# Kernel tuning notes

Hardware: AMD Instinct MI355X
Metric: run time of the kernel (lower is better)

## Reference

```python
import jax, jax.numpy as jnp
import numpy as np

B, LQ, LK, QD, KD, VD, H = 8, 128, 1024, 128, 128, 128, 128
NEG_INF = -1e6  # d2l masked_softmax fill value


def setup_inputs() -> dict:
    key = jax.random.key(0)
    k1, k2, k3, k4, k5, k6, k7 = jax.random.split(key, 7)
    return {
        "queries": jax.random.normal(k1, (B, LQ, QD), dtype=jnp.float32),
        "keys": jax.random.normal(k2, (B, LK, KD), dtype=jnp.float32),
        "values": jax.random.normal(k3, (B, LK, VD), dtype=jnp.float32),
        "valid_lens": jax.random.randint(k4, (B,), 0, LK),
        # learned params: torch Linear(in,out,bias=False); stored here as [in,out]
        "W_q": jax.random.normal(k5, (QD, H), dtype=jnp.float32) / np.sqrt(QD),
        "W_k": jax.random.normal(k6, (KD, H), dtype=jnp.float32) / np.sqrt(KD),
        "w_v": jax.random.normal(k7, (H,), dtype=jnp.float32) / np.sqrt(H),
    }


def reference(queries, keys, values, valid_lens, W_q, W_k, w_v):
    q = jnp.einsum("blq,qh->blh", queries, W_q)            # [B,Lq,H]
    k = jnp.einsum("bsk,kh->bsh", keys, W_k)               # [B,Lk,H]
    features = jnp.tanh(q[:, :, None, :] + k[:, None, :, :])  # [B,Lq,Lk,H]
    scores = jnp.einsum("blsh,h->bls", features, w_v)      # [B,Lq,Lk]
    mask = jnp.arange(LK)[None, None, :] < valid_lens[:, None, None]
    scores = jnp.where(mask, scores, NEG_INF)
    attn = jax.nn.softmax(scores, axis=-1)                 # dropout p=0.0 -> identity
    return jnp.einsum("bls,bsv->blv", attn, values)        # [B,Lq,Vd]
```

## Files before the change

### kernel.cpp

```cpp
#include <hip/hip_runtime.h>
#include <hip/hip_fp16.h>

#define B_   8
#define LQ_  128
#define LK_  1024
#define H_   128

__device__ float        g_eq  [B_ * LQ_ * H_];
__device__ uint4        g_ekT4[B_ * (H_ / 4) * (LK_ / 2)];
__device__ unsigned int g_vh  [B_ * LK_ * (H_ / 2)];

#define C2LOG2E 2.8853900817779268f

__global__ __launch_bounds__(256) void proj_conv(const float* __restrict__ q,
                                                 const float* __restrict__ k,
                                                 const float* __restrict__ Wq,
                                                 const float* __restrict__ Wk,
                                                 const float* __restrict__ values) {
    const int bx = blockIdx.x, ch = blockIdx.y;
    const int t = threadIdx.x;
    if (bx >= 288) {
        const int idx = ((bx - 288) + (ch << 9)) * 256 + t;
        float4 v = *(const float4*)(values + (size_t)idx * 4);
        __half2 p0 = __floats2half2_rn(v.x, v.y);
        __half2 p1 = __floats2half2_rn(v.z, v.w);
        *(uint2*)(g_vh + (size_t)idx * 2) =
            make_uint2(*(unsigned int*)&p0, *(unsigned int*)&p1);
        return;
    }
    __shared__ float Ws[H_ * 64];
    __shared__ float Xs[32 * H_];
    const bool isq = (bx < 32);
    const float* X; const float* W; int r0;
    if (isq) { X = q; W = Wq; r0 = bx * 32; }
    else     { X = k; W = Wk; r0 = (bx - 32) * 32; }

    #pragma unroll
    for (int u = 0; u < 8; ++u) {
        int p = u * 256 + t;
        int kk = p >> 4, c4 = p & 15;
        *(float4*)(Ws + kk * 64 + c4 * 4) = *(const float4*)(W + kk * H_ + ch * 64 + c4 * 4);
    }
    #pragma unroll
    for (int u = 0; u < 4; ++u) {
        int idx = u * 256 + t;
        int r = idx >> 5, c = idx & 31;
        *(float4*)(Xs + r * H_ + c * 4) = *(const float4*)(X + (size_t)(r0 + r) * H_ + c * 4);
    }
    __syncthreads();

    const int rr = t >> 4;
    const int cc = t & 15;
    float acc[2][4] = {};
    #pragma unroll 4
    for (int kk = 0; kk < H_; ++kk) {
        float4 w4 = *(const float4*)(Ws + kk * 64 + cc * 4);
        float x0 = Xs[(rr * 2) * H_ + kk];
        float x1 = Xs[(rr * 2 + 1) * H_ + kk];
        acc[0][0] = fmaf(x0, w4.x, acc[0][0]); acc[0][1] = fmaf(x0, w4.y, acc[0][1]);
        acc[0][2] = fmaf(x0, w4.z, acc[0][2]); acc[0][3] = fmaf(x0, w4.w, acc[0][3]);
        acc[1][0] = fmaf(x1, w4.x, acc[1][0]); acc[1][1] = fmaf(x1, w4.y, acc[1][1]);
        acc[1][2] = fmaf(x1, w4.z, acc[1][2]); acc[1][3] = fmaf(x1, w4.w, acc[1][3]);
    }
    if (isq) {
        #pragma unroll
        for (int i = 0; i < 2; ++i) {
            float4 o;
            o.x = __builtin_amdgcn_exp2f(acc[i][0] * C2LOG2E);
            o.y = __builtin_amdgcn_exp2f(acc[i][1] * C2LOG2E);
            o.z = __builtin_amdgcn_exp2f(acc[i][2] * C2LOG2E);
            o.w = __builtin_amdgcn_exp2f(acc[i][3] * C2LOG2E);
            *(float4*)(g_eq + (size_t)(r0 + rr * 2 + i) * H_ + ch * 64 + cc * 4) = o;
        }
    } else {
        const int b  = r0 >> 10;
        const int s0 = (r0 & 1023) + rr * 2;
        const int h4 = ch * 16 + cc;
        uint4 pk;
        #pragma unroll
        for (int j = 0; j < 4; ++j) {
            float e0 = __builtin_amdgcn_exp2f(acc[0][j] * C2LOG2E);
            float e1 = __builtin_amdgcn_exp2f(acc[1][j] * C2LOG2E);
            __half2 p = __floats2half2_rn(e0, e1);
            ((unsigned int*)&pk)[j] = *(unsigned int*)&p;
        }
        g_ekT4[((size_t)b * (H_ / 4) + h4) * (LK_ / 2) + (s0 >> 1)] = pk;
    }
}

__global__ __launch_bounds__(512, 2) void fused_attn(const int* __restrict__ valid_lens,
                                                     const float* __restrict__ w_v,
                                                     float* __restrict__ out) {
    __shared__ float qs[2][H_];
    __shared__ float wv[H_];
    __shared__ float scA[LK_], scB[LK_];
    __shared__ float sredA[8], sredB[8];
    __shared__ float rinvs[2];
    __shared__ float part[16][2][H_];
    const int t = threadIdx.x;
    const int lane = t & 63, wid = t >> 6;
    const int g = blockIdx.x & 1;
    const int idx = blockIdx.x >> 1;
    const int b = 4 * g + (idx & 3);
    const int l0 = (idx >> 2) * 2;
    int valid = valid_lens[b];
    valid = min(max(valid, 0), LK_);

    if (t < 256) qs[t >> 7][t & 127] = g_eq[(size_t)(b * LQ_ + l0 + (t >> 7)) * H_ + (t & 127)];
    else if (t < 384) wv[t - 256] = w_v[t - 256];
    __syncthreads();

    const int s0 = 2 * t;
    float p0 = 0.0f, p1 = 0.0f;
    if (valid == 0) {
        for (int i = t; i < LK_; i += 512) { scA[i] = 1.0f; scB[i] = 1.0f; }
    } else if (s0 < valid) {
        const uint4* __restrict__ ek = g_ekT4 + (size_t)b * (H_ / 4) * (LK_ / 2) + t;
        float a00 = 0.0f, a01 = 0.0f, a10 = 0.0f, a11 = 0.0f;
        #pragma unroll 4
        for (int h4 = 0; h4 < H_ / 4; ++h4) {
            uint4 u = ek[(size_t)h4 * (LK_ / 2)];
            #pragma unroll
            for (int j = 0; j < 4; ++j) {
                unsigned int uj = ((const unsigned int*)&u)[j];
                float2 ef = __half22float2(*(const __half2*)&uj);
                const int h = h4 * 4 + j;
                const float qa = qs[0][h], qb = qs[1][h], wh = wv[h];
                a00 = fmaf(wh, __builtin_amdgcn_rcpf(fmaf(qa, ef.x, 1.0f)), a00);
                a01 = fmaf(wh, __builtin_amdgcn_rcpf(fmaf(qa, ef.y, 1.0f)), a01);
                a10 = fmaf(wh, __builtin_amdgcn_rcpf(fmaf(qb, ef.x, 1.0f)), a10);
                a11 = fmaf(wh, __builtin_amdgcn_rcpf(fmaf(qb, ef.y, 1.0f)), a11);
            }
        }
        const float cc = -2.0f * 1.44269504f;
        float e00 = __builtin_amdgcn_exp2f(a00 * cc);
        float e01 = __builtin_amdgcn_exp2f(a01 * cc);
        float e10 = __builtin_amdgcn_exp2f(a10 * cc);
        float e11 = __builtin_amdgcn_exp2f(a11 * cc);
        *(float2*)(scA + s0) = make_float2(e00, e01);
        *(float2*)(scB + s0) = make_float2(e10, e11);
        const bool odd_ok = (s0 + 1 < valid);
        p0 = e00 + (odd_ok ? e01 : 0.0f);
        p1 = e10 + (odd_ok ? e11 : 0.0f);
    }
    #pragma unroll
    for (int kk = 32; kk; kk >>= 1) {
        p0 += __shfl_xor(p0, kk, 64);
        p1 += __shfl_xor(p1, kk, 64);
    }
    if (lane == 0) { sredA[wid] = p0; sredB[wid] = p1; }
    __syncthreads();
    if (t < 2) {
        const float* sr = t ? sredB : sredA;
        float s8 = ((sr[0] + sr[1]) + (sr[2] + sr[3]))
                 + ((sr[4] + sr[5]) + (sr[6] + sr[7]));
        rinvs[t] = (valid == 0) ? (1.0f / 1024.0f) : (1.0f / s8);
    }
    __syncthreads();
    const int n = (valid == 0) ? LK_ : valid;

    const int c = t >> 5;
    const int v4 = t & 31;
    const uint2* vb = (const uint2*)g_vh + (size_t)b * LK_ * (H_ / 4) + v4;
    float ax0 = 0.0f, ay0 = 0.0f, az0 = 0.0f, aw0 = 0.0f;
    float ax1 = 0.0f, ay1 = 0.0f, az1 = 0.0f, aw1 = 0.0f;
    #pragma unroll 4
    for (int s = c; s < n; s += 16) {
        uint2 u = vb[(size_t)s * (H_ / 4)];
        float2 v01 = __half22float2(*(const __half2*)&u.x);
        float2 v23 = __half22float2(*(const __half2*)&u.y);
        float w0 = scA[s], w1 = scB[s];
        ax0 = fmaf(w0, v01.x, ax0); ay0 = fmaf(w0, v01.y, ay0);
        az0 = fmaf(w0, v23.x, az0); aw0 = fmaf(w0, v23.y, aw0);
        ax1 = fmaf(w1, v01.x, ax1); ay1 = fmaf(w1, v01.y, ay1);
        az1 = fmaf(w1, v23.x, az1); aw1 = fmaf(w1, v23.y, aw1);
    }
    *(float4*)(&part[c][0][4 * v4]) = make_float4(ax0, ay0, az0, aw0);
    *(float4*)(&part[c][1][4 * v4]) = make_float4(ax1, ay1, az1, aw1);
    __syncthreads();
    if (t < 256) {
        const int rr = t >> 7, v = t & 127;
        float o = 0.0f;
        #pragma unroll
        for (int cc2 = 0; cc2 < 16; ++cc2) o += part[cc2][rr][v];
        out[(size_t)(b * LQ_ + l0 + rr) * H_ + v] = o * rinvs[rr];
    }
}

extern "C" void kernel_launch(void* const* d_in, const int* in_sizes, int n_in,
                              void* d_out, int out_size, void* d_ws, size_t ws_size,
                              hipStream_t stream) {
    const float* queries    = (const float*)d_in[0];
    const float* keys       = (const float*)d_in[1];
    const float* values     = (const float*)d_in[2];
    const int*   valid_lens = (const int*)d_in[3];
    const float* W_q        = (const float*)d_in[4];
    const float* W_k        = (const float*)d_in[5];
    const float* w_v        = (const float*)d_in[6];
    float* out = (float*)d_out;
    (void)d_ws; (void)ws_size; (void)in_sizes; (void)n_in; (void)out_size;

    proj_conv <<<dim3(800, 2), 256, 0, stream>>>(queries, keys, W_q, W_k, values);
    fused_attn<<<512, 512, 0, stream>>>(valid_lens, w_v, out);
}
```

Measured before the change: 36.97 us.

## Split fused attention into separate score and softmax-PV kernels

Breaks the fused attention kernel into a score kernel and a softmax/PV kernel. The score kernel uses one 128-thread block per query row and 256-key chunk and exits early past valid_len, so load balances across the ragged valid lengths. Scores go through a global buffer that the second kernel reads back into shared memory for the reduction and the PV product. This adds an extra launch and a global round trip for the scores, and each score thread now covers only one query row, so it loses the reuse of each key load across two rows.

Measured after the change: 38.02 us. 1.03x slower.

```diff
diff --git a/kernel.cpp b/kernel.cpp
--- a/kernel.cpp
+++ b/kernel.cpp
@@ -9,6 +9,7 @@
 __device__ float        g_eq  [B_ * LQ_ * H_];
 __device__ uint4        g_ekT4[B_ * (H_ / 4) * (LK_ / 2)];
 __device__ unsigned int g_vh  [B_ * LK_ * (H_ / 2)];
+__device__ float        g_sc  [B_ * LQ_ * LK_];
 
 #define C2LOG2E 2.8853900817779268f
 
@@ -88,67 +89,69 @@
     }
 }
 
-__global__ __launch_bounds__(512, 2) void fused_attn(const int* __restrict__ valid_lens,
-                                                     const float* __restrict__ w_v,
-                                                     float* __restrict__ out) {
-    __shared__ float qs[2][H_];
-    __shared__ float wv[H_];
-    __shared__ float scA[LK_], scB[LK_];
+__global__ __launch_bounds__(128) void score_kernel(const int* __restrict__ valid_lens,
+                                                    const float* __restrict__ w_v) {
+    const int row = blockIdx.x;
+    const int b = row >> 7;
+    int valid = valid_lens[b];
+    valid = min(max(valid, 0), LK_);
+    const int sbase = (int)blockIdx.y << 8;
+    if (sbase >= valid) return;
+    const int s0 = sbase + 2 * (int)threadIdx.x;
+    if (s0 >= valid) return;
+
+    const float* __restrict__ q0 = g_eq + (size_t)row * H_;
+    const uint4* __restrict__ ek = g_ekT4 + (size_t)b * (H_ / 4) * (LK_ / 2) + (s0 >> 1);
+    float a0 = 0.0f, a1 = 0.0f;
+    #pragma unroll 4
+    for (int h4 = 0; h4 < H_ / 4; ++h4) {
+        uint4 u = ek[(size_t)h4 * (LK_ / 2)];
+        #pragma unroll
+        for (int j = 0; j < 4; ++j) {
+            unsigned int uj = ((const unsigned int*)&u)[j];
+            float2 ef = __half22float2(*(const __half2*)&uj);
+            const int h = h4 * 4 + j;
+            const float qh = q0[h], wh = w_v[h];
+            a0 = fmaf(wh, __builtin_amdgcn_rcpf(fmaf(qh, ef.x, 1.0f)), a0);
+            a1 = fmaf(wh, __builtin_amdgcn_rcpf(fmaf(qh, ef.y, 1.0f)), a1);
+        }
+    }
+    const float cc = -2.0f * 1.44269504f;
+    float e0 = __builtin_amdgcn_exp2f(a0 * cc);
+    float e1 = __builtin_amdgcn_exp2f(a1 * cc);
+    *(float2*)(g_sc + (size_t)row * LK_ + s0) = make_float2(e0, e1);
+}
+
+__global__ __launch_bounds__(512, 4) void smpv_kernel(const int* __restrict__ valid_lens,
+                                                      float* __restrict__ out) {
+    __shared__ float sA[LK_], sB[LK_];
     __shared__ float sredA[8], sredB[8];
     __shared__ float rinvs[2];
     __shared__ float part[16][2][H_];
     const int t = threadIdx.x;
     const int lane = t & 63, wid = t >> 6;
-    const int g = blockIdx.x & 1;
-    const int idx = blockIdx.x >> 1;
-    const int b = 4 * g + (idx & 3);
-    const int l0 = (idx >> 2) * 2;
+    const int b = blockIdx.x >> 6, l0 = (blockIdx.x & 63) * 2;
     int valid = valid_lens[b];
     valid = min(max(valid, 0), LK_);
 
-    if (t < 256) qs[t >> 7][t & 127] = g_eq[(size_t)(b * LQ_ + l0 + (t >> 7)) * H_ + (t & 127)];
-    else if (t < 384) wv[t - 256] = w_v[t - 256];
-    __syncthreads();
-
-    const int s0 = 2 * t;
-    float p0 = 0.0f, p1 = 0.0f;
+    float pA = 0.0f, pB = 0.0f;
     if (valid == 0) {
-        for (int i = t; i < LK_; i += 512) { scA[i] = 1.0f; scB[i] = 1.0f; }
-    } else if (s0 < valid) {
-        const uint4* __restrict__ ek = g_ekT4 + (size_t)b * (H_ / 4) * (LK_ / 2) + t;
-        float a00 = 0.0f, a01 = 0.0f, a10 = 0.0f, a11 = 0.0f;
-        #pragma unroll 4
-        for (int h4 = 0; h4 < H_ / 4; ++h4) {
-            uint4 u = ek[(size_t)h4 * (LK_ / 2)];
-            #pragma unroll
-            for (int j = 0; j < 4; ++j) {
-                unsigned int uj = ((const unsigned int*)&u)[j];
-                float2 ef = __half22float2(*(const __half2*)&uj);
-                const int h = h4 * 4 + j;
-                const float qa = qs[0][h], qb = qs[1][h], wh = wv[h];
-                a00 = fmaf(wh, __builtin_amdgcn_rcpf(fmaf(qa, ef.x, 1.0f)), a00);
-                a01 = fmaf(wh, __builtin_amdgcn_rcpf(fmaf(qa, ef.y, 1.0f)), a01);
-                a10 = fmaf(wh, __builtin_amdgcn_rcpf(fmaf(qb, ef.x, 1.0f)), a10);
-                a11 = fmaf(wh, __builtin_amdgcn_rcpf(fmaf(qb, ef.y, 1.0f)), a11);
-            }
-        }
-        const float cc = -2.0f * 1.44269504f;
-        float e00 = __builtin_amdgcn_exp2f(a00 * cc);
-        float e01 = __builtin_amdgcn_exp2f(a01 * cc);
-        float e10 = __builtin_amdgcn_exp2f(a10 * cc);
-        float e11 = __builtin_amdgcn_exp2f(a11 * cc);
-        *(float2*)(scA + s0) = make_float2(e00, e01);
-        *(float2*)(scB + s0) = make_float2(e10, e11);
-        const bool odd_ok = (s0 + 1 < valid);
-        p0 = e00 + (odd_ok ? e01 : 0.0f);
-        p1 = e10 + (odd_ok ? e11 : 0.0f);
+        for (int i = t; i < LK_; i += 512) { sA[i] = 1.0f; sB[i] = 1.0f; }
+    } else {
+        const float* __restrict__ srcA = g_sc + (size_t)(b * LQ_ + l0) * LK_;
+        const float* __restrict__ srcB = srcA + LK_;
+        for (int i = t; i < valid; i += 512) {
+            float a = srcA[i], bb = srcB[i];
+            sA[i] = a; sB[i] = bb;
+            pA += a; pB += bb;
+        }
     }
     #pragma unroll
     for (int kk = 32; kk; kk >>= 1) {
-        p0 += __shfl_xor(p0, kk, 64);
-        p1 += __shfl_xor(p1, kk, 64);
-    }
-    if (lane == 0) { sredA[wid] = p0; sredB[wid] = p1; }
+        pA += __shfl_xor(pA, kk, 64);
+        pB += __shfl_xor(pB, kk, 64);
+    }
+    if (lane == 0) { sredA[wid] = pA; sredB[wid] = pB; }
     __syncthreads();
     if (t < 2) {
         const float* sr = t ? sredB : sredA;
@@ -169,7 +172,7 @@
         uint2 u = vb[(size_t)s * (H_ / 4)];
         float2 v01 = __half22float2(*(const __half2*)&u.x);
         float2 v23 = __half22float2(*(const __half2*)&u.y);
-        float w0 = scA[s], w1 = scB[s];
+        float w0 = sA[s], w1 = sB[s];
         ax0 = fmaf(w0, v01.x, ax0); ay0 = fmaf(w0, v01.y, ay0);
         az0 = fmaf(w0, v23.x, az0); aw0 = fmaf(w0, v23.y, aw0);
         ax1 = fmaf(w1, v01.x, ax1); ay1 = fmaf(w1, v01.y, ay1);
@@ -200,6 +203,7 @@
     float* out = (float*)d_out;
     (void)d_ws; (void)ws_size; (void)in_sizes; (void)n_in; (void)out_size;
 
-    proj_conv <<<dim3(800, 2), 256, 0, stream>>>(queries, keys, W_q, W_k, values);
-    fused_attn<<<512, 512, 0, stream>>>(valid_lens, w_v, out);
-}
+    proj_conv   <<<dim3(800, 2), 256, 0, stream>>>(queries, keys, W_q, W_k, values);
+    score_kernel<<<dim3(B_ * LQ_, 4), 128, 0, stream>>>(valid_lens, w_v);
+    smpv_kernel <<<512, 512, 0, stream>>>(valid_lens, out);
+}
```

## Compute scores for all keys unconditionally, drop LDS staging of q and w_v

Applied to the files above, without the earlier changes.

Removes the shared-memory staging of the query row and w_v, reading them directly from global memory (uniform loads) so one barrier disappears. The score loop and the PV loop now run over all 1024 keys, with masked positions given zero weight instead of being skipped. This removes branch divergence and the valid_len-dependent loop bound. It also switches to a plain batch-major block mapping and raises the occupancy hint to 4 blocks per CU. The cost is extra rcp/exp and value-load work for masked keys, which is a large fraction when valid lengths are short.

Measured after the change: 43.33 us. +17.2%, slower.

```diff
diff --git a/kernel.cpp b/kernel.cpp
--- a/kernel.cpp
+++ b/kernel.cpp
@@ -88,61 +88,54 @@
     }
 }
 
-__global__ __launch_bounds__(512, 2) void fused_attn(const int* __restrict__ valid_lens,
+__global__ __launch_bounds__(512, 4) void fused_attn(const int* __restrict__ valid_lens,
                                                      const float* __restrict__ w_v,
                                                      float* __restrict__ out) {
-    __shared__ float qs[2][H_];
-    __shared__ float wv[H_];
     __shared__ float scA[LK_], scB[LK_];
     __shared__ float sredA[8], sredB[8];
     __shared__ float rinvs[2];
     __shared__ float part[16][2][H_];
     const int t = threadIdx.x;
     const int lane = t & 63, wid = t >> 6;
-    const int g = blockIdx.x & 1;
-    const int idx = blockIdx.x >> 1;
-    const int b = 4 * g + (idx & 3);
-    const int l0 = (idx >> 2) * 2;
+    const int b = blockIdx.x >> 6, l0 = (blockIdx.x & 63) * 2;
     int valid = valid_lens[b];
     valid = min(max(valid, 0), LK_);
 
-    if (t < 256) qs[t >> 7][t & 127] = g_eq[(size_t)(b * LQ_ + l0 + (t >> 7)) * H_ + (t & 127)];
-    else if (t < 384) wv[t - 256] = w_v[t - 256];
-    __syncthreads();
+    const int s0 = 2 * t;
+    const float* __restrict__ q0 = g_eq + (size_t)(b * LQ_ + l0) * H_;
+    const float* __restrict__ q1 = q0 + H_;
+    const uint4* __restrict__ ek = g_ekT4 + (size_t)b * (H_ / 4) * (LK_ / 2) + t;
+    float a00 = 0.0f, a01 = 0.0f, a10 = 0.0f, a11 = 0.0f;
+    #pragma unroll 4
+    for (int h4 = 0; h4 < H_ / 4; ++h4) {
+        uint4 u = ek[(size_t)h4 * (LK_ / 2)];
+        #pragma unroll
+        for (int j = 0; j < 4; ++j) {
+            unsigned int uj = ((const unsigned int*)&u)[j];
+            float2 ef = __half22float2(*(const __half2*)&uj);
+            const int h = h4 * 4 + j;
+            const float qa = q0[h], qb = q1[h], wh = w_v[h];
+            a00 = fmaf(wh, __builtin_amdgcn_rcpf(fmaf(qa, ef.x, 1.0f)), a00);
+            a01 = fmaf(wh, __builtin_amdgcn_rcpf(fmaf(qa, ef.y, 1.0f)), a01);
+            a10 = fmaf(wh, __builtin_amdgcn_rcpf(fmaf(qb, ef.x, 1.0f)), a10);
+            a11 = fmaf(wh, __builtin_amdgcn_rcpf(fmaf(qb, ef.y, 1.0f)), a11);
+        }
+    }
+    const float cexp = -2.0f * 1.44269504f;
+    float e00 = __builtin_amdgcn_exp2f(a00 * cexp);
+    float e01 = __builtin_amdgcn_exp2f(a01 * cexp);
+    float e10 = __builtin_amdgcn_exp2f(a10 * cexp);
+    float e11 = __builtin_amdgcn_exp2f(a11 * cexp);
+    const bool uni = (valid == 0);
+    const bool ok0 = s0 < valid, ok1 = s0 + 1 < valid;
+    float w00 = uni ? 1.0f : (ok0 ? e00 : 0.0f);
+    float w01 = uni ? 1.0f : (ok1 ? e01 : 0.0f);
+    float w10 = uni ? 1.0f : (ok0 ? e10 : 0.0f);
+    float w11 = uni ? 1.0f : (ok1 ? e11 : 0.0f);
+    *(float2*)(scA + s0) = make_float2(w00, w01);
+    *(float2*)(scB + s0) = make_float2(w10, w11);
+    float p0 = w00 + w01, p1 = w10 + w11;
 
-    const int s0 = 2 * t;
-    float p0 = 0.0f, p1 = 0.0f;
-    if (valid == 0) {
-        for (int i = t; i < LK_; i += 512) { scA[i] = 1.0f; scB[i] = 1.0f; }
-    } else if (s0 < valid) {
-        const uint4* __restrict__ ek = g_ekT4 + (size_t)b * (H_ / 4) * (LK_ / 2) + t;
-        float a00 = 0.0f, a01 = 0.0f, a10 = 0.0f, a11 = 0.0f;
-        #pragma unroll 4
-        for (int h4 = 0; h4 < H_ / 4; ++h4) {
-            uint4 u = ek[(size_t)h4 * (LK_ / 2)];
-            #pragma unroll
-            for (int j = 0; j < 4; ++j) {
-                unsigned int uj = ((const unsigned int*)&u)[j];
-                float2 ef = __half22float2(*(const __half2*)&uj);
-                const int h = h4 * 4 + j;
-                const float qa = qs[0][h], qb = qs[1][h], wh = wv[h];
-                a00 = fmaf(wh, __builtin_amdgcn_rcpf(fmaf(qa, ef.x, 1.0f)), a00);
-                a01 = fmaf(wh, __builtin_amdgcn_rcpf(fmaf(qa, ef.y, 1.0f)), a01);
-                a10 = fmaf(wh, __builtin_amdgcn_rcpf(fmaf(qb, ef.x, 1.0f)), a10);
-                a11 = fmaf(wh, __builtin_amdgcn_rcpf(fmaf(qb, ef.y, 1.0f)), a11);
-            }
-        }
-        const float cc = -2.0f * 1.44269504f;
-        float e00 = __builtin_amdgcn_exp2f(a00 * cc);
-        float e01 = __builtin_amdgcn_exp2f(a01 * cc);
-        float e10 = __builtin_amdgcn_exp2f(a10 * cc);
-        float e11 = __builtin_amdgcn_exp2f(a11 * cc);
-        *(float2*)(scA + s0) = make_float2(e00, e01);
-        *(float2*)(scB + s0) = make_float2(e10, e11);
-        const bool odd_ok = (s0 + 1 < valid);
-        p0 = e00 + (odd_ok ? e01 : 0.0f);
-        p1 = e10 + (odd_ok ? e11 : 0.0f);
-    }
     #pragma unroll
     for (int kk = 32; kk; kk >>= 1) {
         p0 += __shfl_xor(p0, kk, 64);
@@ -154,10 +147,9 @@
         const float* sr = t ? sredB : sredA;
         float s8 = ((sr[0] + sr[1]) + (sr[2] + sr[3]))
                  + ((sr[4] + sr[5]) + (sr[6] + sr[7]));
-        rinvs[t] = (valid == 0) ? (1.0f / 1024.0f) : (1.0f / s8);
+        rinvs[t] = 1.0f / s8;
     }
     __syncthreads();
-    const int n = (valid == 0) ? LK_ : valid;
 
     const int c = t >> 5;
     const int v4 = t & 31;
@@ -165,7 +157,7 @@
     float ax0 = 0.0f, ay0 = 0.0f, az0 = 0.0f, aw0 = 0.0f;
     float ax1 = 0.0f, ay1 = 0.0f, az1 = 0.0f, aw1 = 0.0f;
     #pragma unroll 4
-    for (int s = c; s < n; s += 16) {
+    for (int s = c; s < LK_; s += 16) {
         uint2 u = vb[(size_t)s * (H_ / 4)];
         float2 v01 = __half22float2(*(const __half2*)&u.x);
         float2 v23 = __half22float2(*(const __half2*)&u.y);
```
